# Kernel tuning notes

Measured on AMD Instinct MI355X. Metric: run time of the kernel, lower is better.

Reference implementation:

```python
import jax, jax.numpy as jnp
import numpy as np

N_PITCH, N_DUR, N_TIME, N_VEL = 128, 160, 100, 128
VOCAB = N_PITCH + N_DUR + N_TIME + N_VEL  # 516
B, S = 32, 2048


def _build_vocab_tables():
    # token_type: 0='p', 1='d', 2='t', 3='v'; token_value: numeric suffix of itos_vocab[i]
    tt = np.concatenate([
        np.full(N_PITCH, 0), np.full(N_DUR, 1), np.full(N_TIME, 2), np.full(N_VEL, 3)
    ]).astype(np.int32)
    tv = np.concatenate([
        np.arange(N_PITCH), np.arange(N_DUR), np.arange(N_TIME), np.arange(N_VEL)
    ]).astype(np.float32)
    return jnp.asarray(tt), jnp.asarray(tv)


def setup_inputs() -> dict:
    key = jax.random.key(0)
    k1, k2, k3, k4 = jax.random.split(key, 4)
    token_type, token_value = _build_vocab_tables()
    return {
        "output": jax.random.normal(k1, (B, VOCAB, S), dtype=jnp.float32),
        "target": jax.random.randint(k2, (B, S), 0, VOCAB, dtype=jnp.int32),
        "token_type": token_type,
        "token_value": token_value,
        "coeff": jnp.asarray([0.5, 0.6, 0.2, 0.2], dtype=jnp.float32),
        "harmonic": jnp.asarray([0.6, 0.6, 0.2, 0.2, 0.2, 0.2, 1.5], dtype=jnp.float32),
    }


def _penalty_mask(pred, target, token_type, token_value, coeff, harmonic):
    pt, tt = token_type[pred], token_type[target]      # [B,S] type codes
    pv, tv = token_value[pred], token_value[target]    # [B,S] numeric values
    d = jnp.abs(pv - tv)
    # pitch: harmonic-interval weights (values are integer-valued floats -> exact ==)
    pitch_w = jnp.where(d == 7, harmonic[0],
              jnp.where(d == 5, harmonic[1],
              jnp.where(d == 3, harmonic[2],
              jnp.where(d == 4, harmonic[3],
              jnp.where(d == 1, harmonic[4],
              jnp.where(d == 2, harmonic[5], harmonic[6]))))))
    dur_w = coeff[1] * d / 160.0
    time_w = coeff[2] * d / 100.0
    vel_w = coeff[3] * d / 128.0
    same_type_w = jnp.where(pt == 0, pitch_w,
                  jnp.where(pt == 1, dur_w,
                  jnp.where(pt == 2, time_w, vel_w)))
    return jnp.where(pt != tt, coeff[0], same_type_w)


def reference(output, target, token_type, token_value, coeff, harmonic):
    # Faithful to original: softmax over last (seq) axis, then argmax over vocab axis 1
    sm = jax.nn.softmax(output, axis=-1)
    pred = jnp.argmax(sm, axis=1)                      # [B,S]
    # mean cross-entropy over B*S (class axis = 1)
    logp = jax.nn.log_softmax(output, axis=1)          # [B,V,S]
    nll = -jnp.take_along_axis(logp, target[:, None, :], axis=1)[:, 0, :]
    loss = nll.mean()
    mask = _penalty_mask(pred, target, token_type, token_value, coeff, harmonic)
    high_cost = (loss * mask).mean()
    return loss + high_cost
```

## Files before the change

kernel.cpp:

```cpp
#include <hip/hip_runtime.h>

#define BB 32
#define SS 2048
#define VV 516
#define NBS (BB * SS)
#define NCHUNK 16
#define NPART 256

__device__ inline float waveReduceSum(float v) {
    #pragma unroll
    for (int o = 32; o > 0; o >>= 1) v += __shfl_down(v, o, 64);
    return v;
}

__global__ __launch_bounds__(256) void hl_tile(const float* __restrict__ x,
                                               const int* __restrict__ target,
                                               int* __restrict__ ctr,
                                               float* __restrict__ pSum,
                                               float* __restrict__ pBest,
                                               int* __restrict__ pIdx,
                                               float* __restrict__ xtArr) {
    __shared__ float ldsX[8 * 2048];
    __shared__ float sLse[8];

    if (blockIdx.x == 0 && threadIdx.x == 0) ctr[0] = 0;

    const int c = blockIdx.x & 15, b = blockIdx.x >> 4;
    const int v0 = 32 * c + (c > 12 ? c - 12 : 0);
    const int nv = (c >= 12) ? 33 : 32;
    const int tid = threadIdx.x, lane = tid & 63, wv = tid >> 6;

    const int s0 = tid << 2;
    const int bs = b * SS + s0;
    int4 tgA = *(const int4*)(target + bs);
    int4 tgB = *(const int4*)(target + bs + 1024);
    int tg[8] = {tgA.x, tgA.y, tgA.z, tgA.w, tgB.x, tgB.y, tgB.z, tgB.w};

    float sum[8], best[8], xt[8];
    int bi[8];
    #pragma unroll
    for (int i = 0; i < 8; ++i) { sum[i] = 0.f; best[i] = -1e30f; bi[i] = v0; xt[i] = 0.f; }

    const float* xb = x + (size_t)(b * VV + v0) * SS;

    for (int vs = 0; vs < nv; vs += 8) {
        int m = nv - vs; if (m > 8) m = 8;
        #pragma unroll
        for (int k = 0; k < 2; ++k) {
            int lr = wv * 2 + k;
            if (lr < m) {
                const float* row = xb + (size_t)(vs + lr) * SS;
                float4 v[8];
                #pragma unroll
                for (int j = 0; j < 8; ++j)
                    v[j] = *(const float4*)(row + j * 256 + lane * 4);
                float a0 = 0.f, a1 = 0.f, a2 = 0.f, a3 = 0.f;
                #pragma unroll
                for (int j = 0; j < 8; ++j) {
                    *(float4*)(ldsX + lr * 2048 + j * 256 + lane * 4) = v[j];
                    a0 += __expf(v[j].x); a1 += __expf(v[j].y);
                    a2 += __expf(v[j].z); a3 += __expf(v[j].w);
                }
                float ssum = waveReduceSum((a0 + a1) + (a2 + a3));
                if (lane == 0) sLse[lr] = __logf(ssum);
            }
        }
        __syncthreads();
        for (int v = 0; v < m; ++v) {
            float l = sLse[v];
            int vg = v0 + vs + v;
            float4 xa = *(const float4*)(ldsX + v * 2048 + s0);
            float4 xc = *(const float4*)(ldsX + v * 2048 + 1024 + s0);
            float e[8] = {xa.x, xa.y, xa.z, xa.w, xc.x, xc.y, xc.z, xc.w};
            #pragma unroll
            for (int i = 0; i < 8; ++i) {
                sum[i] += __expf(e[i]);
                float sc = e[i] - l;
                if (sc > best[i]) { best[i] = sc; bi[i] = vg; }
                if (vg == tg[i]) xt[i] = e[i];
            }
        }
        __syncthreads();
    }

    int o = c * NBS + bs;
    *(float4*)(pSum + o)         = make_float4(sum[0], sum[1], sum[2], sum[3]);
    *(float4*)(pSum + o + 1024)  = make_float4(sum[4], sum[5], sum[6], sum[7]);
    *(float4*)(pBest + o)        = make_float4(best[0], best[1], best[2], best[3]);
    *(float4*)(pBest + o + 1024) = make_float4(best[4], best[5], best[6], best[7]);
    *(int4*)(pIdx + o)           = make_int4(bi[0], bi[1], bi[2], bi[3]);
    *(int4*)(pIdx + o + 1024)    = make_int4(bi[4], bi[5], bi[6], bi[7]);
    int v1 = v0 + nv;
    #pragma unroll
    for (int i = 0; i < 8; ++i) {
        int col = (i < 4) ? (s0 + i) : (1024 + s0 + i - 4);
        if (tg[i] >= v0 && tg[i] < v1) xtArr[b * SS + col] = xt[i];
    }
}

__global__ __launch_bounds__(256) void hl_comb(const int* __restrict__ target,
                                               const int* __restrict__ ttype,
                                               const float* __restrict__ tval,
                                               const float* __restrict__ coeff,
                                               const float* __restrict__ harm,
                                               const float* __restrict__ pSum,
                                               const float* __restrict__ pBest,
                                               const int* __restrict__ pIdx,
                                               const float* __restrict__ xtArr,
                                               float* __restrict__ pNll,
                                               float* __restrict__ pMask,
                                               int* __restrict__ counter,
                                               float* __restrict__ outv) {
    __shared__ float lds[8];
    __shared__ bool isLast;
    int idx = blockIdx.x * 256 + threadIdx.x;

    float sum = 0.f, best = -1e30f;
    int bestIdx = 0;
    #pragma unroll
    for (int c = 0; c < NCHUNK; ++c) {
        int o = c * NBS + idx;
        sum += pSum[o];
        float sc = pBest[o];
        int ii = pIdx[o];
        if (sc > best) { best = sc; bestIdx = ii; }
    }
    int tgt = target[idx];
    float nll = __logf(sum) - xtArr[idx];

    int pt = ttype[bestIdx], tt = ttype[tgt];
    float pv = tval[bestIdx], tv = tval[tgt];
    float d = fabsf(pv - tv);
    float pw = (d == 7.f) ? harm[0] : (d == 5.f) ? harm[1] : (d == 3.f) ? harm[2]
             : (d == 4.f) ? harm[3] : (d == 1.f) ? harm[4] : (d == 2.f) ? harm[5]
             : harm[6];
    float w = (pt == 0) ? pw
            : (pt == 1) ? coeff[1] * d * (1.f / 160.f)
            : (pt == 2) ? coeff[2] * d * (1.f / 100.f)
            :             coeff[3] * d * (1.f / 128.f);
    float mask = (pt != tt) ? coeff[0] : w;

    int lane = threadIdx.x & 63, wvv = threadIdx.x >> 6;
    float rn = waveReduceSum(nll);
    if (lane == 0) lds[wvv] = rn;
    __syncthreads();
    float totN = (threadIdx.x == 0) ? lds[0] + lds[1] + lds[2] + lds[3] : 0.f;
    __syncthreads();
    float rm = waveReduceSum(mask);
    if (lane == 0) lds[wvv] = rm;
    __syncthreads();
    if (threadIdx.x == 0) {
        pNll[blockIdx.x]  = totN;
        pMask[blockIdx.x] = lds[0] + lds[1] + lds[2] + lds[3];
        __threadfence();
        unsigned old = atomicAdd((unsigned*)counter, 1u);
        isLast = (old == NPART - 1);
    }
    __syncthreads();
    if (isLast) {
        __threadfence();
        int t = threadIdx.x;
        float n = waveReduceSum(pNll[t]);
        float m = waveReduceSum(pMask[t]);
        if (lane == 0) { lds[wvv] = n; lds[4 + wvv] = m; }
        __syncthreads();
        if (t == 0) {
            float tn = lds[0] + lds[1] + lds[2] + lds[3];
            float tm = lds[4] + lds[5] + lds[6] + lds[7];
            const float inv = 1.f / (float)NBS;
            outv[0] = (tn * inv) * (1.f + tm * inv);
        }
    }
}

extern "C" void kernel_launch(void* const* d_in, const int* in_sizes, int n_in,
                              void* d_out, int out_size, void* d_ws, size_t ws_size,
                              hipStream_t stream) {
    const float* x      = (const float*)d_in[0];
    const int*   target = (const int*)d_in[1];
    const int*   ttype  = (const int*)d_in[2];
    const float* tval   = (const float*)d_in[3];
    const float* coeff  = (const float*)d_in[4];
    const float* harm   = (const float*)d_in[5];

    float* ws    = (float*)d_ws;
    int*   ctr   = (int*)ws;
    float* pNll  = ws + 4;
    float* pMask = pNll + NPART;
    float* xtArr = pMask + NPART;
    float* pSum  = xtArr + NBS;
    float* pBest = pSum + (size_t)NCHUNK * NBS;
    int*   pIdx  = (int*)(pBest + (size_t)NCHUNK * NBS);

    hl_tile<<<BB * NCHUNK, 256, 0, stream>>>(x, target, ctr, pSum, pBest,
                                             pIdx, xtArr);
    hl_comb<<<NBS / 256, 256, 0, stream>>>(target, ttype, tval, coeff, harm,
                                           pSum, pBest, pIdx, xtArr,
                                           pNll, pMask, ctr, (float*)d_out);
}
```

Baseline: 48.85 us.

## Store exponentials in LDS and double threads per block in tile kernel

Each loaded row is exponentiated once and stored in LDS, so the per-column pass reuses those values instead of recomputing exp. Argmax uses multiplication by the reciprocal row sum rather than subtracting a log-sum. The target logit is recovered as the log of the stored exponential. Blocks now use 512 threads with one row per wave and four columns per thread, raising parallelism per block. The trade-off is a small precision change in the target logit and possible overflow of exp for large inputs.

```diff
diff --git a/kernel.cpp b/kernel.cpp
--- a/kernel.cpp
+++ b/kernel.cpp
@@ -13,15 +13,15 @@
     return v;
 }
 
-__global__ __launch_bounds__(256) void hl_tile(const float* __restrict__ x,
-                                               const int* __restrict__ target,
-                                               int* __restrict__ ctr,
-                                               float* __restrict__ pSum,
-                                               float* __restrict__ pBest,
-                                               int* __restrict__ pIdx,
-                                               float* __restrict__ xtArr) {
-    __shared__ float ldsX[8 * 2048];
-    __shared__ float sLse[8];
+__global__ __launch_bounds__(512, 4) void hl_tile(const float* __restrict__ x,
+                                                  const int* __restrict__ target,
+                                                  int* __restrict__ ctr,
+                                                  float* __restrict__ pSum,
+                                                  float* __restrict__ pBest,
+                                                  int* __restrict__ pIdx,
+                                                  float* __restrict__ xtArr) {
+    __shared__ float ldsE[8 * 2048];
+    __shared__ float sRcp[8];
 
     if (blockIdx.x == 0 && threadIdx.x == 0) ctr[0] = 0;
 
@@ -32,70 +32,65 @@
 
     const int s0 = tid << 2;
     const int bs = b * SS + s0;
-    int4 tgA = *(const int4*)(target + bs);
-    int4 tgB = *(const int4*)(target + bs + 1024);
-    int tg[8] = {tgA.x, tgA.y, tgA.z, tgA.w, tgB.x, tgB.y, tgB.z, tgB.w};
+    int4 tg4 = *(const int4*)(target + bs);
+    int tg[4] = {tg4.x, tg4.y, tg4.z, tg4.w};
 
-    float sum[8], best[8], xt[8];
-    int bi[8];
+    float sum[4], best[4], xt[4];
+    int bi[4];
     #pragma unroll
-    for (int i = 0; i < 8; ++i) { sum[i] = 0.f; best[i] = -1e30f; bi[i] = v0; xt[i] = 0.f; }
+    for (int i = 0; i < 4; ++i) { sum[i] = 0.f; best[i] = -1.f; bi[i] = v0; xt[i] = 0.f; }
 
     const float* xb = x + (size_t)(b * VV + v0) * SS;
 
     for (int vs = 0; vs < nv; vs += 8) {
         int m = nv - vs; if (m > 8) m = 8;
-        #pragma unroll
-        for (int k = 0; k < 2; ++k) {
-            int lr = wv * 2 + k;
-            if (lr < m) {
-                const float* row = xb + (size_t)(vs + lr) * SS;
-                float4 v[8];
-                #pragma unroll
-                for (int j = 0; j < 8; ++j)
-                    v[j] = *(const float4*)(row + j * 256 + lane * 4);
-                float a0 = 0.f, a1 = 0.f, a2 = 0.f, a3 = 0.f;
-                #pragma unroll
-                for (int j = 0; j < 8; ++j) {
-                    *(float4*)(ldsX + lr * 2048 + j * 256 + lane * 4) = v[j];
-                    a0 += __expf(v[j].x); a1 += __expf(v[j].y);
-                    a2 += __expf(v[j].z); a3 += __expf(v[j].w);
-                }
-                float ssum = waveReduceSum((a0 + a1) + (a2 + a3));
-                if (lane == 0) sLse[lr] = __logf(ssum);
+        if (wv < m) {
+            const float* row = xb + (size_t)(vs + wv) * SS;
+            float4 v[8];
+            #pragma unroll
+            for (int j = 0; j < 8; ++j)
+                v[j] = *(const float4*)(row + j * 256 + lane * 4);
+            float a0 = 0.f, a1 = 0.f, a2 = 0.f, a3 = 0.f;
+            #pragma unroll
+            for (int j = 0; j < 8; ++j) {
+                float4 e;
+                e.x = __expf(v[j].x); e.y = __expf(v[j].y);
+                e.z = __expf(v[j].z); e.w = __expf(v[j].w);
+                *(float4*)(ldsE + wv * 2048 + j * 256 + lane * 4) = e;
+                a0 += e.x; a1 += e.y; a2 += e.z; a3 += e.w;
             }
+            float ssum = waveReduceSum((a0 + a1) + (a2 + a3));
+            if (lane == 0) sRcp[wv] = 1.f / ssum;
         }
         __syncthreads();
         for (int v = 0; v < m; ++v) {
-            float l = sLse[v];
+            float r = sRcp[v];
             int vg = v0 + vs + v;
-            float4 xa = *(const float4*)(ldsX + v * 2048 + s0);
-            float4 xc = *(const float4*)(ldsX + v * 2048 + 1024 + s0);
-            float e[8] = {xa.x, xa.y, xa.z, xa.w, xc.x, xc.y, xc.z, xc.w};
+            float4 e4 = *(const float4*)(ldsE + v * 2048 + s0);
+            float e[4] = {e4.x, e4.y, e4.z, e4.w};
             #pragma unroll
-            for (int i = 0; i < 8; ++i) {
-                sum[i] += __expf(e[i]);
-                float sc = e[i] - l;
+            for (int i = 0; i < 4; ++i) {
+                sum[i] += e[i];
+                float sc = e[i] * r;
                 if (sc > best[i]) { best[i] = sc; bi[i] = vg; }
-                if (vg == tg[i]) xt[i] = e[i];
             }
+        }
+        #pragma unroll
+        for (int i = 0; i < 4; ++i) {
+            int lr = tg[i] - (v0 + vs);
+            if (lr >= 0 && lr < m) xt[i] = __logf(ldsE[lr * 2048 + s0 + i]);
         }
         __syncthreads();
     }
 
     int o = c * NBS + bs;
-    *(float4*)(pSum + o)         = make_float4(sum[0], sum[1], sum[2], sum[3]);
-    *(float4*)(pSum + o + 1024)  = make_float4(sum[4], sum[5], sum[6], sum[7]);
-    *(float4*)(pBest + o)        = make_float4(best[0], best[1], best[2], best[3]);
-    *(float4*)(pBest + o + 1024) = make_float4(best[4], best[5], best[6], best[7]);
-    *(int4*)(pIdx + o)           = make_int4(bi[0], bi[1], bi[2], bi[3]);
-    *(int4*)(pIdx + o + 1024)    = make_int4(bi[4], bi[5], bi[6], bi[7]);
+    *(float4*)(pSum + o)  = make_float4(sum[0], sum[1], sum[2], sum[3]);
+    *(float4*)(pBest + o) = make_float4(best[0], best[1], best[2], best[3]);
+    *(int4*)(pIdx + o)    = make_int4(bi[0], bi[1], bi[2], bi[3]);
     int v1 = v0 + nv;
     #pragma unroll
-    for (int i = 0; i < 8; ++i) {
-        int col = (i < 4) ? (s0 + i) : (1024 + s0 + i - 4);
-        if (tg[i] >= v0 && tg[i] < v1) xtArr[b * SS + col] = xt[i];
-    }
+    for (int i = 0; i < 4; ++i)
+        if (tg[i] >= v0 && tg[i] < v1) xtArr[bs + i] = xt[i];
 }
 
 __global__ __launch_bounds__(256) void hl_comb(const int* __restrict__ target,
@@ -192,7 +187,7 @@
     float* pBest = pSum + (size_t)NCHUNK * NBS;
     int*   pIdx  = (int*)(pBest + (size_t)NCHUNK * NBS);
 
-    hl_tile<<<BB * NCHUNK, 256, 0, stream>>>(x, target, ctr, pSum, pBest,
+    hl_tile<<<BB * NCHUNK, 512, 0, stream>>>(x, target, ctr, pSum, pBest,
                                              pIdx, xtArr);
     hl_comb<<<NBS / 256, 256, 0, stream>>>(target, ttype, tval, coeff, harm,
                                            pSum, pBest, pIdx, xtArr,
```

After: 46.98 us. -3.8%, faster.
